# Kernel tuning notes

Measured on AMD Instinct MI355X. Metric: run time of the kernel, lower is better.

Reference implementation:

```python
import jax, jax.numpy as jnp
import numpy as np


def setup_inputs() -> dict:
    key = jax.random.key(0)
    k = jax.random.split(key, 5)
    bs, n_heads, ch, n_obj, emb = 4, 8, 64, 8, 64
    ih = iw = 32
    T = ih * iw
    return {
        "qkv": jax.random.normal(k[0], (bs, 3 * n_heads * ch, T), dtype=jnp.float32),
        "bboxes": jax.random.uniform(k[1], (bs, n_obj, 5), dtype=jnp.float32),
        "null_prompt_emb": jax.random.normal(k[2], (bs, emb, T), dtype=jnp.float32),
        "prompt_emb": jax.random.normal(k[3], (bs, emb, T), dtype=jnp.float32),
        "W_prompt": jax.random.normal(k[4], (3 * n_heads * ch, emb), dtype=jnp.float32) * 0.02,
        "n_heads": n_heads,
        "image_h": ih,
        "image_w": iw,
    }


def _region_masks(bboxes, h, w):
    # Faithful translation of get_region: bbox unpacked as (x, y, width, height, obj_idx).
    # Returns float masks [b, n_obj, h*w].
    x, y, bw, bh = bboxes[..., 0], bboxes[..., 1], bboxes[..., 2], bboxes[..., 3]
    i0 = jnp.minimum(float(h) - 1.0, jnp.floor(y * h))
    j0 = jnp.minimum(float(w) - 1.0, jnp.floor(x * w))
    i1 = i0 + jnp.maximum(1.0, jnp.ceil(bh * h))
    j1 = j0 + jnp.maximum(1.0, jnp.ceil(bw * w))
    ii = jnp.arange(h, dtype=jnp.float32)
    jj = jnp.arange(w, dtype=jnp.float32)
    mi = (ii >= i0[..., None]) & (ii < i1[..., None])          # [b, n, h]
    mj = (jj >= j0[..., None]) & (jj < j1[..., None])          # [b, n, w]
    m = (mi[..., :, None] & mj[..., None, :]).astype(jnp.float32)  # [b, n, h, w]
    return m.reshape(m.shape[0], m.shape[1], h * w)


def reference(qkv, bboxes, null_prompt_emb, prompt_emb, W_prompt, n_heads, image_h, image_w):
    bs, width, T = qkv.shape
    ch = width // (3 * n_heads)
    scale = float(ch) ** -0.25  # 1/sqrt(sqrt(ch))

    def split3(x):
        x = x.reshape(bs * n_heads, 3 * ch, T)
        return x[:, :ch], x[:, ch:2 * ch], x[:, 2 * ch:]

    q, k, v = split3(qkv)
    # to_prompt_token is a 1x1 Conv1d (no bias) == matmul over the channel dim
    nq, nk, nv = split3(jnp.einsum('oc,bct->bot', W_prompt, null_prompt_emb))
    pq, pk, pv = split3(jnp.einsum('oc,bct->bot', W_prompt, prompt_emb))

    def attn(qh, kh, vh, col_mask=None):
        w = jnp.einsum('bct,bcs->bts', qh * scale, kh * scale)
        if col_mask is not None:
            w = jnp.where(col_mask[:, None, :] > 0.5, w, -1e9)
        w = jax.nn.softmax(w.astype(jnp.float32), axis=-1).astype(qh.dtype)
        return jnp.einsum('bts,bcs->btc', w, vh)  # [bs*heads, T, ch]

    # global (null-prompt) attention
    a_null = attn(q + nq, k + nk, v + nv)

    # per-object masked attention, blended by region masks
    masks = _region_masks(bboxes, image_h, image_w)       # [bs, n_obj, T]
    masks = jnp.repeat(masks, n_heads, axis=0)            # [(bs*heads), n_obj, T]
    qf, kf, vf = q + pq, k + pk, v + pv
    a_fg = jnp.zeros_like(a_null)
    counter = jnp.zeros((bs * n_heads, T, 1), dtype=jnp.float32)
    for o in range(masks.shape[1]):  # small fixed loop over objects
        m = masks[:, o]                                   # [bs*heads, T]
        a_fg = a_fg + m[:, :, None] * attn(qf, kf, vf, col_mask=m)
        counter = counter + m[:, :, None]
    fg = counter > 0.5
    a_final = jnp.where(fg, a_fg, a_null) / jnp.where(fg, counter, 1.0)
    return jnp.transpose(a_final, (0, 2, 1)).reshape(bs, n_heads * ch, T)
```

## Files before the change

kernel.cpp:

```cpp
#include <hip/hip_runtime.h>

#define BS 4
#define NH 8
#define TT 1024
#define WROWS 1536
#define NOBJ 8
#define NT 65536

#define QNT_OFF  0
#define KNT_OFF  2097152
#define VNCS_OFF 4194304
#define QFT_OFF  6291456
#define KFT_OFF  8388608
#define VFT_OFF  10485760

typedef __attribute__((ext_vector_type(8))) short short8;
typedef __attribute__((ext_vector_type(4))) float v4f;

__device__ __forceinline__ short f2bf(float f) {
    unsigned u = __float_as_uint(f);
    u = (u + 0x7FFF + ((u >> 16) & 1)) >> 16;
    return (short)u;
}
__device__ __forceinline__ unsigned cvtpk(float a, float b) {
    unsigned u;
    asm("v_cvt_pk_bf16_f32 %0, %1, %2" : "=v"(u) : "v"(a), "v"(b));
    return u;
}
__device__ __forceinline__ float fexp2(float x) {
    float r;
    asm("v_exp_f32 %0, %1" : "=v"(r) : "v"(x));
    return r;
}
__device__ __forceinline__ int pi64(int s) { return 4 * (s & 15) + (s >> 4); }

__device__ __forceinline__ void get_region(const float* __restrict__ bb,
                                           int& i0, int& j0, int& hh, int& ww) {
    float x = bb[0], y = bb[1], bw = bb[2], bh = bb[3];
    float i0f = fminf(31.0f, floorf(y * 32.0f));
    float j0f = fminf(31.0f, floorf(x * 32.0f));
    float i1f = i0f + fmaxf(1.0f, ceilf(bh * 32.0f));
    float j1f = j0f + fmaxf(1.0f, ceilf(bw * 32.0f));
    i0 = (int)i0f; j0 = (int)j0f;
    int i1 = min(32, (int)i1f);
    int j1 = min(32, (int)j1f);
    hh = i1 - i0; ww = j1 - j0;
}

__global__ __launch_bounds__(256)
void fuse_kernel(const float* __restrict__ qkv, const float* __restrict__ nEmb,
                 const float* __restrict__ pEmb, const float* __restrict__ W,
                 short* __restrict__ wsS) {
    __shared__ float WtT[64][68];
    __shared__ float En[64][64];
    __shared__ float Ep[64][64];
    short* sbuf = (short*)&WtT[0][0];
    int t0 = blockIdx.x * 64;
    int r0 = blockIdx.y * 64;
    int b  = blockIdx.z;
    int tid = threadIdx.x;
    int half = tid >> 4;
    int q4 = (tid & 15) * 4;
#pragma unroll
    for (int p = 0; p < 4; ++p) {
        int rr = p * 16 + half;
        float4 w4 = *(const float4*)&W[(r0 + rr) * 64 + q4];
        WtT[q4 + 0][rr] = w4.x; WtT[q4 + 1][rr] = w4.y;
        WtT[q4 + 2][rr] = w4.z; WtT[q4 + 3][rr] = w4.w;
        int e = p * 16 + half;
        *(float4*)&En[e][q4] = *(const float4*)&nEmb[(b * 64 + e) * TT + t0 + q4];
        *(float4*)&Ep[e][q4] = *(const float4*)&pEmb[(b * 64 + e) * TT + t0 + q4];
    }
    __syncthreads();
    int tr = tid >> 4, tc = tid & 15;
    float an[4][4] = {{0.f}}, ap[4][4] = {{0.f}};
#pragma unroll 8
    for (int e = 0; e < 64; ++e) {
        float4 w4 = *(const float4*)&WtT[e][tr * 4];
        float4 n4 = *(const float4*)&En[e][tc * 4];
        float4 p4 = *(const float4*)&Ep[e][tc * 4];
        float w[4]  = {w4.x, w4.y, w4.z, w4.w};
        float nn[4] = {n4.x, n4.y, n4.z, n4.w};
        float pp[4] = {p4.x, p4.y, p4.z, p4.w};
#pragma unroll
        for (int i = 0; i < 4; ++i)
#pragma unroll
            for (int j = 0; j < 4; ++j) {
                an[i][j] += w[i] * nn[j];
                ap[i][j] += w[i] * pp[j];
            }
    }
    int sec = (r0 % 192) / 64;
    int h = r0 / 192, bh = b * 8 + h;
    float sc = (sec == 0) ? 0.18033688f : 1.0f;
#pragma unroll
    for (int i = 0; i < 4; ++i) {
        int r = r0 + tr * 4 + i;
        float4 x4 = *(const float4*)&qkv[(b * WROWS + r) * TT + t0 + tc * 4];
        an[i][0] = (an[i][0] + x4.x) * sc; an[i][1] = (an[i][1] + x4.y) * sc;
        an[i][2] = (an[i][2] + x4.z) * sc; an[i][3] = (an[i][3] + x4.w) * sc;
        ap[i][0] = (ap[i][0] + x4.x) * sc; ap[i][1] = (ap[i][1] + x4.y) * sc;
        ap[i][2] = (ap[i][2] + x4.z) * sc; ap[i][3] = (ap[i][3] + x4.w) * sc;
    }
    if (sec == 2) {
        short* Vn = wsS + VNCS_OFF + bh * NT;
        __syncthreads();
#pragma unroll
        for (int i = 0; i < 4; ++i)
#pragma unroll
            for (int j = 0; j < 4; ++j) {
                int p = tc * 4 + j;
                sbuf[(tr * 4 + i) * 72 + pi64(p)] = f2bf(an[i][j]);
            }
        __syncthreads();
#pragma unroll
        for (int rep = 0; rep < 2; ++rep) {
            int idx = rep * 256 + tid; int cl = idx >> 3, c8 = idx & 7;
            *(short8*)&Vn[cl * TT + t0 + c8 * 8] = *(const short8*)&sbuf[cl * 72 + c8 * 8];
        }
        short* dst = wsS + VFT_OFF + bh * NT + t0 * 64;
        __syncthreads();
#pragma unroll
        for (int j = 0; j < 4; ++j) {
            uint2 u; u.x = cvtpk(ap[0][j], ap[1][j]); u.y = cvtpk(ap[2][j], ap[3][j]);
            *(uint2*)&sbuf[(tc * 4 + j) * 72 + tr * 4] = u;
        }
        __syncthreads();
#pragma unroll
        for (int rep = 0; rep < 2; ++rep) {
            int idx = rep * 256 + tid; int tl = idx >> 3, c8 = idx & 7;
            *(short8*)&dst[tl * 64 + c8 * 8] = *(const short8*)&sbuf[tl * 72 + c8 * 8];
        }
    } else {
        short* dn = wsS + (sec == 0 ? QNT_OFF : KNT_OFF) + bh * NT + t0 * 64;
        short* df = wsS + (sec == 0 ? QFT_OFF : KFT_OFF) + bh * NT + t0 * 64;
        __syncthreads();
#pragma unroll
        for (int j = 0; j < 4; ++j) {
            uint2 u; u.x = cvtpk(an[0][j], an[1][j]); u.y = cvtpk(an[2][j], an[3][j]);
            *(uint2*)&sbuf[(tc * 4 + j) * 72 + tr * 4] = u;
        }
        __syncthreads();
#pragma unroll
        for (int rep = 0; rep < 2; ++rep) {
            int idx = rep * 256 + tid; int tl = idx >> 3, c8 = idx & 7;
            *(short8*)&dn[tl * 64 + c8 * 8] = *(const short8*)&sbuf[tl * 72 + c8 * 8];
        }
        __syncthreads();
#pragma unroll
        for (int j = 0; j < 4; ++j) {
            uint2 u; u.x = cvtpk(ap[0][j], ap[1][j]); u.y = cvtpk(ap[2][j], ap[3][j]);
            *(uint2*)&sbuf[(tc * 4 + j) * 72 + tr * 4] = u;
        }
        __syncthreads();
#pragma unroll
        for (int rep = 0; rep < 2; ++rep) {
            int idx = rep * 256 + tid; int tl = idx >> 3, c8 = idx & 7;
            *(short8*)&df[tl * 64 + c8 * 8] = *(const short8*)&sbuf[tl * 72 + c8 * 8];
        }
    }
}

__global__ __launch_bounds__(256)
void attn_fused(const short* __restrict__ wsS, const float* __restrict__ bboxes,
                float* __restrict__ out) {
    __shared__ __align__(16) short lds[13824];
    __shared__ unsigned short tmap[1024];
    short* Qs = lds;
    short* Ks = lds + 4608;
    short* Vs = lds + 9216;
    int rt = blockIdx.x, bh = blockIdx.y;
    int b = bh >> 3, h = bh & 7;
    int t0 = rt * 64;
    int tid = threadIdx.x;
    int w = tid >> 6, lane = tid & 63, ln = lane & 15, qd = lane >> 4;
    const short* QnT = wsS + QNT_OFF + bh * NT;
    const short* KnT = wsS + KNT_OFF + bh * NT;
    const short* Vn  = wsS + VNCS_OFF + bh * NT;
    const short* QfT = wsS + QFT_OFF + bh * NT;
    const short* KfT = wsS + KFT_OFF + bh * NT;
    const short* VfT = wsS + VFT_OFF + bh * NT;
    int sidx = tid, scell = sidx >> 3, sc8 = sidx & 7;
    int sidx2 = 256 + tid, scell2 = sidx2 >> 3, sc82 = sidx2 & 7;

    *(short8*)&Qs[scell * 72 + sc8 * 8]  = *(const short8*)&QnT[(t0 + scell) * 64 + sc8 * 8];
    *(short8*)&Qs[scell2 * 72 + sc82 * 8] = *(const short8*)&QnT[(t0 + scell2) * 64 + sc82 * 8];
    __syncthreads();
    short8 aq0 = *(const short8*)&Qs[(16 * w + ln) * 72 + qd * 8];
    short8 aq1 = *(const short8*)&Qs[(16 * w + ln) * 72 + 32 + qd * 8];
    v4f O[4]; float l[4];
#pragma unroll
    for (int r = 0; r < 4; ++r) l[r] = 0.f;
#pragma unroll
    for (int cc = 0; cc < 4; ++cc) O[cc] = (v4f){0.f, 0.f, 0.f, 0.f};
    short8 kreg[2], vreg[2];
    kreg[0] = *(const short8*)&KnT[scell * 64 + sc8 * 8];
    kreg[1] = *(const short8*)&KnT[scell2 * 64 + sc82 * 8];
    vreg[0] = *(const short8*)&Vn[scell * TT + sc8 * 8];
    vreg[1] = *(const short8*)&Vn[scell2 * TT + sc82 * 8];
    for (int ct = 0; ct < 16; ++ct) {
        __syncthreads();
        *(short8*)&Ks[scell * 72 + sc8 * 8]  = kreg[0];
        *(short8*)&Ks[scell2 * 72 + sc82 * 8] = kreg[1];
        *(short8*)&Vs[scell * 72 + sc8 * 8]  = vreg[0];
        *(short8*)&Vs[scell2 * 72 + sc82 * 8] = vreg[1];
        __syncthreads();
        if (ct < 15) {
            int s0 = (ct + 1) * 64;
            kreg[0] = *(const short8*)&KnT[(s0 + scell) * 64 + sc8 * 8];
            kreg[1] = *(const short8*)&KnT[(s0 + scell2) * 64 + sc82 * 8];
            vreg[0] = *(const short8*)&Vn[scell * TT + s0 + sc8 * 8];
            vreg[1] = *(const short8*)&Vn[scell2 * TT + s0 + sc82 * 8];
        }
        v4f S[4];
#pragma unroll
        for (int nn = 0; nn < 4; ++nn) {
            short8 b0 = *(const short8*)&Ks[(nn * 16 + ln) * 72 + qd * 8];
            short8 b1 = *(const short8*)&Ks[(nn * 16 + ln) * 72 + 32 + qd * 8];
            v4f z = (v4f){0.f, 0.f, 0.f, 0.f};
            z = __builtin_amdgcn_mfma_f32_16x16x32_bf16(aq0, b0, z, 0, 0, 0);
            z = __builtin_amdgcn_mfma_f32_16x16x32_bf16(aq1, b1, z, 0, 0, 0);
            S[nn] = z;
        }
#pragma unroll
        for (int r = 0; r < 4; ++r) {
            float e0 = fexp2(S[0][r]);
            float e1 = fexp2(S[1][r]);
            float e2 = fexp2(S[2][r]);
            float e3 = fexp2(S[3][r]);
            l[r] += (e0 + e1) + (e2 + e3);
            uint2 u; u.x = cvtpk(e0, e1); u.y = cvtpk(e2, e3);
            *(uint2*)&Qs[(w * 16 + 4 * qd + r) * 72 + 4 * ln] = u;
        }
        short8 ap0 = *(const short8*)&Qs[(w * 16 + ln) * 72 + qd * 8];
        short8 ap1 = *(const short8*)&Qs[(w * 16 + ln) * 72 + 32 + qd * 8];
#pragma unroll
        for (int cc = 0; cc < 4; ++cc) {
            short8 bv0 = *(const short8*)&Vs[(cc * 16 + ln) * 72 + qd * 8];
            short8 bv1 = *(const short8*)&Vs[(cc * 16 + ln) * 72 + 32 + qd * 8];
            O[cc] = __builtin_amdgcn_mfma_f32_16x16x32_bf16(ap0, bv0, O[cc], 0, 0, 0);
            O[cc] = __builtin_amdgcn_mfma_f32_16x16x32_bf16(ap1, bv1, O[cc], 0, 0, 0);
        }
    }
    v4f Onull[4];
#pragma unroll
    for (int r = 0; r < 4; ++r) {
        float rs = l[r];
        rs += __shfl_xor(rs, 1, 64);
        rs += __shfl_xor(rs, 2, 64);
        rs += __shfl_xor(rs, 4, 64);
        rs += __shfl_xor(rs, 8, 64);
        float inv = 1.0f / rs;
#pragma unroll
        for (int cc = 0; cc < 4; ++cc) Onull[cc][r] = O[cc][r] * inv;
    }

    __syncthreads();
    *(short8*)&Qs[scell * 72 + sc8 * 8]  = *(const short8*)&QfT[(t0 + scell) * 64 + sc8 * 8];
    *(short8*)&Qs[scell2 * 72 + sc82 * 8] = *(const short8*)&QfT[(t0 + scell2) * 64 + sc82 * 8];
    __syncthreads();
    aq0 = *(const short8*)&Qs[(16 * w + ln) * 72 + qd * 8];
    aq1 = *(const short8*)&Qs[(16 * w + ln) * 72 + 32 + qd * 8];
    v4f Oacc[4]; float cnt[4];
#pragma unroll
    for (int r = 0; r < 4; ++r) cnt[r] = 0.f;
#pragma unroll
    for (int cc = 0; cc < 4; ++cc) Oacc[cc] = (v4f){0.f, 0.f, 0.f, 0.f};

    for (int o = 0; o < NOBJ; ++o) {
        int i0, j0, hh, ww;
        get_region(&bboxes[(b * NOBJ + o) * 5], i0, j0, hh, ww);
        int i1 = i0 + hh;
        if (i0 > 2 * rt + 1 || i1 <= 2 * rt) continue;
        int R = hh * ww;
        for (int idx = tid; idx < R; idx += 256) {
            int ri = idx / ww; int rj = idx - ri * ww;
            tmap[idx] = (unsigned short)((i0 + ri) * 32 + j0 + rj);
        }
        __syncthreads();
#pragma unroll
        for (int r = 0; r < 4; ++r) l[r] = 0.f;
#pragma unroll
        for (int cc = 0; cc < 4; ++cc) O[cc] = (v4f){0.f, 0.f, 0.f, 0.f};
        int nct = (R + 63) >> 6;
        {
            int tA = tmap[min(scell, R - 1)];
            int tB = tmap[min(scell2, R - 1)];
            kreg[0] = *(const short8*)&KfT[tA * 64 + sc8 * 8];
            kreg[1] = *(const short8*)&KfT[tB * 64 + sc82 * 8];
            vreg[0] = *(const short8*)&VfT[tA * 64 + sc8 * 8];
            vreg[1] = *(const short8*)&VfT[tB * 64 + sc82 * 8];
        }
        int pA = pi64(scell), pB = pi64(scell2);
        for (int ct = 0; ct < nct; ++ct) {
            int sb = ct * 64;
            __syncthreads();
            *(short8*)&Ks[scell * 72 + sc8 * 8]  = kreg[0];
            *(short8*)&Ks[scell2 * 72 + sc82 * 8] = kreg[1];
#pragma unroll
            for (int jj = 0; jj < 8; ++jj) {
                int j = (jj + sc8) & 7;
                Vs[(sc8 * 8 + j) * 72 + pA] = vreg[0][j];
            }
#pragma unroll
            for (int jj = 0; jj < 8; ++jj) {
                int j = (jj + sc82) & 7;
                Vs[(sc82 * 8 + j) * 72 + pB] = vreg[1][j];
            }
            __syncthreads();
            if (ct + 1 < nct) {
                int s0 = sb + 64;
                int tA = tmap[min(s0 + scell, R - 1)];
                int tB = tmap[min(s0 + scell2, R - 1)];
                kreg[0] = *(const short8*)&KfT[tA * 64 + sc8 * 8];
                kreg[1] = *(const short8*)&KfT[tB * 64 + sc82 * 8];
                vreg[0] = *(const short8*)&VfT[tA * 64 + sc8 * 8];
                vreg[1] = *(const short8*)&VfT[tB * 64 + sc82 * 8];
            }
            v4f S[4];
#pragma unroll
            for (int nn = 0; nn < 4; ++nn) {
                short8 b0 = *(const short8*)&Ks[(nn * 16 + ln) * 72 + qd * 8];
                short8 b1 = *(const short8*)&Ks[(nn * 16 + ln) * 72 + 32 + qd * 8];
                v4f z = (v4f){0.f, 0.f, 0.f, 0.f};
                z = __builtin_amdgcn_mfma_f32_16x16x32_bf16(aq0, b0, z, 0, 0, 0);
                z = __builtin_amdgcn_mfma_f32_16x16x32_bf16(aq1, b1, z, 0, 0, 0);
                S[nn] = z;
            }
            float v0 = (sb +  0 + ln) < R ? 1.f : 0.f;
            float v1 = (sb + 16 + ln) < R ? 1.f : 0.f;
            float v2 = (sb + 32 + ln) < R ? 1.f : 0.f;
            float v3 = (sb + 48 + ln) < R ? 1.f : 0.f;
#pragma unroll
            for (int r = 0; r < 4; ++r) {
                float e0 = fexp2(S[0][r]) * v0;
                float e1 = fexp2(S[1][r]) * v1;
                float e2 = fexp2(S[2][r]) * v2;
                float e3 = fexp2(S[3][r]) * v3;
                l[r] += (e0 + e1) + (e2 + e3);
                uint2 u; u.x = cvtpk(e0, e1); u.y = cvtpk(e2, e3);
                *(uint2*)&Qs[(w * 16 + 4 * qd + r) * 72 + 4 * ln] = u;
            }
            short8 ap0 = *(const short8*)&Qs[(w * 16 + ln) * 72 + qd * 8];
            short8 ap1 = *(const short8*)&Qs[(w * 16 + ln) * 72 + 32 + qd * 8];
#pragma unroll
            for (int cc = 0; cc < 4; ++cc) {
                short8 bv0 = *(const short8*)&Vs[(cc * 16 + ln) * 72 + qd * 8];
                short8 bv1 = *(const short8*)&Vs[(cc * 16 + ln) * 72 + 32 + qd * 8];
                O[cc] = __builtin_amdgcn_mfma_f32_16x16x32_bf16(ap0, bv0, O[cc], 0, 0, 0);
                O[cc] = __builtin_amdgcn_mfma_f32_16x16x32_bf16(ap1, bv1, O[cc], 0, 0, 0);
            }
        }
#pragma unroll
        for (int r = 0; r < 4; ++r) {
            float rs = l[r];
            rs += __shfl_xor(rs, 1, 64);
            rs += __shfl_xor(rs, 2, 64);
            rs += __shfl_xor(rs, 4, 64);
            rs += __shfl_xor(rs, 8, 64);
            float inv = 1.0f / rs;
            int t = t0 + 16 * w + 4 * qd + r;
            int ti = t >> 5, tj = t & 31;
            bool in = (ti >= i0) && (ti < i1) && (tj >= j0) && (tj < j0 + ww);
            if (in) {
                cnt[r] += 1.f;
#pragma unroll
                for (int cc = 0; cc < 4; ++cc) Oacc[cc][r] += O[cc][r] * inv;
            }
        }
    }

    __syncthreads();
    float* Ot = (float*)lds;
#pragma unroll
    for (int r = 0; r < 4; ++r) {
        int tl = 16 * w + 4 * qd + r;
        float icnt = cnt[r] > 0.f ? 1.0f / cnt[r] : 0.f;
#pragma unroll
        for (int cc = 0; cc < 4; ++cc) {
            float val = cnt[r] > 0.f ? Oacc[cc][r] * icnt : Onull[cc][r];
            Ot[(cc * 16 + ln) * 68 + tl] = val;
        }
    }
    __syncthreads();
    int obase = (b * 512 + h * 64) * TT + t0;
#pragma unroll
    for (int rep = 0; rep < 4; ++rep) {
        int idx = rep * 256 + tid; int c = idx >> 4, t4 = (idx & 15) * 4;
        *(float4*)&out[obase + c * TT + t4] = *(float4*)&Ot[c * 68 + t4];
    }
}

extern "C" void kernel_launch(void* const* d_in, const int* in_sizes, int n_in,
                              void* d_out, int out_size, void* d_ws, size_t ws_size,
                              hipStream_t stream) {
    const float* qkv    = (const float*)d_in[0];
    const float* bboxes = (const float*)d_in[1];
    const float* nEmb   = (const float*)d_in[2];
    const float* pEmb   = (const float*)d_in[3];
    const float* W      = (const float*)d_in[4];
    short* wsS = (short*)d_ws;
    float* out = (float*)d_out;

    fuse_kernel<<<dim3(16, 24, 4), 256, 0, stream>>>(qkv, nEmb, pEmb, W, wsS);
    attn_fused<<<dim3(16, 32), 256, 0, stream>>>(wsS, bboxes, out);
}
```

Before: 154.4 us.

## Shrink attention tiles to one image row and load K/V fragments directly from global

Each attention block now covers 32 query tokens (one image row) with 128 threads instead of 64 tokens with 256, so the grid holds twice as many blocks. The null-prompt pass reads Q, K and V MFMA fragments straight from global memory instead of staging them in LDS, which removes the per-tile barriers. The masked object pass gathers K directly through the token map and double-buffers only the transposed V tile in LDS. The region test becomes a column-only check, since a block's tokens all lie in one row. The cost is more redundant global and L2 traffic, because each wave re-reads K and V without sharing them through LDS.

```diff
diff --git a/kernel.cpp b/kernel.cpp
--- a/kernel.cpp
+++ b/kernel.cpp
@@ -161,62 +161,45 @@
     }
 }
 
-__global__ __launch_bounds__(256)
+__global__ __launch_bounds__(128)
 void attn_fused(const short* __restrict__ wsS, const float* __restrict__ bboxes,
                 float* __restrict__ out) {
-    __shared__ __align__(16) short lds[13824];
+    __shared__ __align__(16) short lds[11520];
     __shared__ unsigned short tmap[1024];
-    short* Qs = lds;
-    short* Ks = lds + 4608;
-    short* Vs = lds + 9216;
-    int rt = blockIdx.x, bh = blockIdx.y;
+    short* Ps = lds;
+    short* Vb = lds + 2304;
+    float* Ot = (float*)(lds + 2304);
+
+    int bh = blockIdx.x, rt = blockIdx.y;
     int b = bh >> 3, h = bh & 7;
-    int t0 = rt * 64;
+    int t0 = rt * 32;
     int tid = threadIdx.x;
-    int w = tid >> 6, lane = tid & 63, ln = lane & 15, qd = lane >> 4;
+    int w = tid >> 6;
+    int lane = tid & 63, ln = lane & 15, qd = lane >> 4;
+    int rB = tid >> 3, c8 = tid & 7;
+
     const short* QnT = wsS + QNT_OFF + bh * NT;
     const short* KnT = wsS + KNT_OFF + bh * NT;
     const short* Vn  = wsS + VNCS_OFF + bh * NT;
     const short* QfT = wsS + QFT_OFF + bh * NT;
     const short* KfT = wsS + KFT_OFF + bh * NT;
     const short* VfT = wsS + VFT_OFF + bh * NT;
-    int sidx = tid, scell = sidx >> 3, sc8 = sidx & 7;
-    int sidx2 = 256 + tid, scell2 = sidx2 >> 3, sc82 = sidx2 & 7;
-
-    *(short8*)&Qs[scell * 72 + sc8 * 8]  = *(const short8*)&QnT[(t0 + scell) * 64 + sc8 * 8];
-    *(short8*)&Qs[scell2 * 72 + sc82 * 8] = *(const short8*)&QnT[(t0 + scell2) * 64 + sc82 * 8];
-    __syncthreads();
-    short8 aq0 = *(const short8*)&Qs[(16 * w + ln) * 72 + qd * 8];
-    short8 aq1 = *(const short8*)&Qs[(16 * w + ln) * 72 + 32 + qd * 8];
+
+    short8 aq0 = *(const short8*)&QnT[(t0 + 16 * w + ln) * 64 + qd * 8];
+    short8 aq1 = *(const short8*)&QnT[(t0 + 16 * w + ln) * 64 + 32 + qd * 8];
     v4f O[4]; float l[4];
 #pragma unroll
     for (int r = 0; r < 4; ++r) l[r] = 0.f;
 #pragma unroll
     for (int cc = 0; cc < 4; ++cc) O[cc] = (v4f){0.f, 0.f, 0.f, 0.f};
-    short8 kreg[2], vreg[2];
-    kreg[0] = *(const short8*)&KnT[scell * 64 + sc8 * 8];
-    kreg[1] = *(const short8*)&KnT[scell2 * 64 + sc82 * 8];
-    vreg[0] = *(const short8*)&Vn[scell * TT + sc8 * 8];
-    vreg[1] = *(const short8*)&Vn[scell2 * TT + sc82 * 8];
     for (int ct = 0; ct < 16; ++ct) {
-        __syncthreads();
-        *(short8*)&Ks[scell * 72 + sc8 * 8]  = kreg[0];
-        *(short8*)&Ks[scell2 * 72 + sc82 * 8] = kreg[1];
-        *(short8*)&Vs[scell * 72 + sc8 * 8]  = vreg[0];
-        *(short8*)&Vs[scell2 * 72 + sc82 * 8] = vreg[1];
-        __syncthreads();
-        if (ct < 15) {
-            int s0 = (ct + 1) * 64;
-            kreg[0] = *(const short8*)&KnT[(s0 + scell) * 64 + sc8 * 8];
-            kreg[1] = *(const short8*)&KnT[(s0 + scell2) * 64 + sc82 * 8];
-            vreg[0] = *(const short8*)&Vn[scell * TT + s0 + sc8 * 8];
-            vreg[1] = *(const short8*)&Vn[scell2 * TT + s0 + sc82 * 8];
-        }
+        int s0 = ct * 64;
         v4f S[4];
 #pragma unroll
         for (int nn = 0; nn < 4; ++nn) {
-            short8 b0 = *(const short8*)&Ks[(nn * 16 + ln) * 72 + qd * 8];
-            short8 b1 = *(const short8*)&Ks[(nn * 16 + ln) * 72 + 32 + qd * 8];
+            const short* kp = &KnT[(s0 + nn * 16 + ln) * 64 + qd * 8];
+            short8 b0 = *(const short8*)kp;
+            short8 b1 = *(const short8*)(kp + 32);
             v4f z = (v4f){0.f, 0.f, 0.f, 0.f};
             z = __builtin_amdgcn_mfma_f32_16x16x32_bf16(aq0, b0, z, 0, 0, 0);
             z = __builtin_amdgcn_mfma_f32_16x16x32_bf16(aq1, b1, z, 0, 0, 0);
@@ -230,14 +213,15 @@
             float e3 = fexp2(S[3][r]);
             l[r] += (e0 + e1) + (e2 + e3);
             uint2 u; u.x = cvtpk(e0, e1); u.y = cvtpk(e2, e3);
-            *(uint2*)&Qs[(w * 16 + 4 * qd + r) * 72 + 4 * ln] = u;
-        }
-        short8 ap0 = *(const short8*)&Qs[(w * 16 + ln) * 72 + qd * 8];
-        short8 ap1 = *(const short8*)&Qs[(w * 16 + ln) * 72 + 32 + qd * 8];
+            *(uint2*)&Ps[(w * 16 + 4 * qd + r) * 72 + 4 * ln] = u;
+        }
+        short8 ap0 = *(const short8*)&Ps[(w * 16 + ln) * 72 + qd * 8];
+        short8 ap1 = *(const short8*)&Ps[(w * 16 + ln) * 72 + 32 + qd * 8];
 #pragma unroll
         for (int cc = 0; cc < 4; ++cc) {
-            short8 bv0 = *(const short8*)&Vs[(cc * 16 + ln) * 72 + qd * 8];
-            short8 bv1 = *(const short8*)&Vs[(cc * 16 + ln) * 72 + 32 + qd * 8];
+            const short* vp = &Vn[(cc * 16 + ln) * TT + s0 + qd * 8];
+            short8 bv0 = *(const short8*)vp;
+            short8 bv1 = *(const short8*)(vp + 32);
             O[cc] = __builtin_amdgcn_mfma_f32_16x16x32_bf16(ap0, bv0, O[cc], 0, 0, 0);
             O[cc] = __builtin_amdgcn_mfma_f32_16x16x32_bf16(ap1, bv1, O[cc], 0, 0, 0);
         }
@@ -255,12 +239,8 @@
         for (int cc = 0; cc < 4; ++cc) Onull[cc][r] = O[cc][r] * inv;
     }
 
-    __syncthreads();
-    *(short8*)&Qs[scell * 72 + sc8 * 8]  = *(const short8*)&QfT[(t0 + scell) * 64 + sc8 * 8];
-    *(short8*)&Qs[scell2 * 72 + sc82 * 8] = *(const short8*)&QfT[(t0 + scell2) * 64 + sc82 * 8];
-    __syncthreads();
-    aq0 = *(const short8*)&Qs[(16 * w + ln) * 72 + qd * 8];
-    aq1 = *(const short8*)&Qs[(16 * w + ln) * 72 + 32 + qd * 8];
+    aq0 = *(const short8*)&QfT[(t0 + 16 * w + ln) * 64 + qd * 8];
+    aq1 = *(const short8*)&QfT[(t0 + 16 * w + ln) * 64 + 32 + qd * 8];
     v4f Oacc[4]; float cnt[4];
 #pragma unroll
     for (int r = 0; r < 4; ++r) cnt[r] = 0.f;
@@ -271,9 +251,9 @@
         int i0, j0, hh, ww;
         get_region(&bboxes[(b * NOBJ + o) * 5], i0, j0, hh, ww);
         int i1 = i0 + hh;
-        if (i0 > 2 * rt + 1 || i1 <= 2 * rt) continue;
+        if (i0 > rt || i1 <= rt) continue;
         int R = hh * ww;
-        for (int idx = tid; idx < R; idx += 256) {
+        for (int idx = tid; idx < R; idx += 128) {
             int ri = idx / ww; int rj = idx - ri * ww;
             tmap[idx] = (unsigned short)((i0 + ri) * 32 + j0 + rj);
         }
@@ -283,45 +263,53 @@
 #pragma unroll
         for (int cc = 0; cc < 4; ++cc) O[cc] = (v4f){0.f, 0.f, 0.f, 0.f};
         int nct = (R + 63) >> 6;
-        {
-            int tA = tmap[min(scell, R - 1)];
-            int tB = tmap[min(scell2, R - 1)];
-            kreg[0] = *(const short8*)&KfT[tA * 64 + sc8 * 8];
-            kreg[1] = *(const short8*)&KfT[tB * 64 + sc82 * 8];
-            vreg[0] = *(const short8*)&VfT[tA * 64 + sc8 * 8];
-            vreg[1] = *(const short8*)&VfT[tB * 64 + sc82 * 8];
-        }
-        int pA = pi64(scell), pB = pi64(scell2);
-        for (int ct = 0; ct < nct; ++ct) {
-            int sb = ct * 64;
-            __syncthreads();
-            *(short8*)&Ks[scell * 72 + sc8 * 8]  = kreg[0];
-            *(short8*)&Ks[scell2 * 72 + sc82 * 8] = kreg[1];
+        short8 vreg[4];
+#pragma unroll
+        for (int k = 0; k < 4; ++k)
+            vreg[k] = *(const short8*)&VfT[(int)tmap[min(rB + 16 * k, R - 1)] * 64 + c8 * 8];
+#pragma unroll
+        for (int k = 0; k < 4; ++k) {
+            int pK = 4 * rB + k;
 #pragma unroll
             for (int jj = 0; jj < 8; ++jj) {
-                int j = (jj + sc8) & 7;
-                Vs[(sc8 * 8 + j) * 72 + pA] = vreg[0][j];
-            }
-#pragma unroll
-            for (int jj = 0; jj < 8; ++jj) {
-                int j = (jj + sc82) & 7;
-                Vs[(sc82 * 8 + j) * 72 + pB] = vreg[1][j];
-            }
-            __syncthreads();
-            if (ct + 1 < nct) {
-                int s0 = sb + 64;
-                int tA = tmap[min(s0 + scell, R - 1)];
-                int tB = tmap[min(s0 + scell2, R - 1)];
-                kreg[0] = *(const short8*)&KfT[tA * 64 + sc8 * 8];
-                kreg[1] = *(const short8*)&KfT[tB * 64 + sc82 * 8];
-                vreg[0] = *(const short8*)&VfT[tA * 64 + sc8 * 8];
-                vreg[1] = *(const short8*)&VfT[tB * 64 + sc82 * 8];
+                int j = (jj + c8) & 7;
+                Vb[(c8 * 8 + j) * 72 + pK] = vreg[k][j];
+            }
+        }
+        if (nct > 1) {
+#pragma unroll
+            for (int k = 0; k < 4; ++k)
+                vreg[k] = *(const short8*)&VfT[(int)tmap[min(64 + rB + 16 * k, R - 1)] * 64 + c8 * 8];
+        }
+        __syncthreads();
+        for (int p = 0; p < nct; ++p) {
+            int sb = p * 64;
+            const short* curV = Vb + (p & 1) * 4608;
+            if (p + 1 < nct) {
+                short* nxtV = Vb + ((p + 1) & 1) * 4608;
+#pragma unroll
+                for (int k = 0; k < 4; ++k) {
+                    int pK = 4 * rB + k;
+#pragma unroll
+                    for (int jj = 0; jj < 8; ++jj) {
+                        int j = (jj + c8) & 7;
+                        nxtV[(c8 * 8 + j) * 72 + pK] = vreg[k][j];
+                    }
+                }
+            }
+            if (p + 2 < nct) {
+                int s0 = sb + 128;
+#pragma unroll
+                for (int k = 0; k < 4; ++k)
+                    vreg[k] = *(const short8*)&VfT[(int)tmap[min(s0 + rB + 16 * k, R - 1)] * 64 + c8 * 8];
             }
             v4f S[4];
 #pragma unroll
             for (int nn = 0; nn < 4; ++nn) {
-                short8 b0 = *(const short8*)&Ks[(nn * 16 + ln) * 72 + qd * 8];
-                short8 b1 = *(const short8*)&Ks[(nn * 16 + ln) * 72 + 32 + qd * 8];
+                int tg = tmap[min(sb + nn * 16 + ln, R - 1)];
+                const short* kp = &KfT[tg * 64 + qd * 8];
+                short8 b0 = *(const short8*)kp;
+                short8 b1 = *(const short8*)(kp + 32);
                 v4f z = (v4f){0.f, 0.f, 0.f, 0.f};
                 z = __builtin_amdgcn_mfma_f32_16x16x32_bf16(aq0, b0, z, 0, 0, 0);
                 z = __builtin_amdgcn_mfma_f32_16x16x32_bf16(aq1, b1, z, 0, 0, 0);
@@ -339,17 +327,18 @@
                 float e3 = fexp2(S[3][r]) * v3;
                 l[r] += (e0 + e1) + (e2 + e3);
                 uint2 u; u.x = cvtpk(e0, e1); u.y = cvtpk(e2, e3);
-                *(uint2*)&Qs[(w * 16 + 4 * qd + r) * 72 + 4 * ln] = u;
-            }
-            short8 ap0 = *(const short8*)&Qs[(w * 16 + ln) * 72 + qd * 8];
-            short8 ap1 = *(const short8*)&Qs[(w * 16 + ln) * 72 + 32 + qd * 8];
+                *(uint2*)&Ps[(w * 16 + 4 * qd + r) * 72 + 4 * ln] = u;
+            }
+            short8 ap0 = *(const short8*)&Ps[(w * 16 + ln) * 72 + qd * 8];
+            short8 ap1 = *(const short8*)&Ps[(w * 16 + ln) * 72 + 32 + qd * 8];
 #pragma unroll
             for (int cc = 0; cc < 4; ++cc) {
-                short8 bv0 = *(const short8*)&Vs[(cc * 16 + ln) * 72 + qd * 8];
-                short8 bv1 = *(const short8*)&Vs[(cc * 16 + ln) * 72 + 32 + qd * 8];
+                short8 bv0 = *(const short8*)&curV[(cc * 16 + ln) * 72 + qd * 8];
+                short8 bv1 = *(const short8*)&curV[(cc * 16 + ln) * 72 + 32 + qd * 8];
                 O[cc] = __builtin_amdgcn_mfma_f32_16x16x32_bf16(ap0, bv0, O[cc], 0, 0, 0);
                 O[cc] = __builtin_amdgcn_mfma_f32_16x16x32_bf16(ap1, bv1, O[cc], 0, 0, 0);
             }
+            __syncthreads();
         }
 #pragma unroll
         for (int r = 0; r < 4; ++r) {
@@ -359,9 +348,8 @@
             rs += __shfl_xor(rs, 4, 64);
             rs += __shfl_xor(rs, 8, 64);
             float inv = 1.0f / rs;
-            int t = t0 + 16 * w + 4 * qd + r;
-            int ti = t >> 5, tj = t & 31;
-            bool in = (ti >= i0) && (ti < i1) && (tj >= j0) && (tj < j0 + ww);
+            int tj = (16 * w + 4 * qd + r) & 31;
+            bool in = (tj >= j0) && (tj < j0 + ww);
             if (in) {
                 cnt[r] += 1.f;
 #pragma unroll
@@ -371,7 +359,6 @@
     }
 
     __syncthreads();
-    float* Ot = (float*)lds;
 #pragma unroll
     for (int r = 0; r < 4; ++r) {
         int tl = 16 * w + 4 * qd + r;
@@ -379,15 +366,15 @@
 #pragma unroll
         for (int cc = 0; cc < 4; ++cc) {
             float val = cnt[r] > 0.f ? Oacc[cc][r] * icnt : Onull[cc][r];
-            Ot[(cc * 16 + ln) * 68 + tl] = val;
+            Ot[(cc * 16 + ln) * 36 + tl] = val;
         }
     }
     __syncthreads();
     int obase = (b * 512 + h * 64) * TT + t0;
 #pragma unroll
     for (int rep = 0; rep < 4; ++rep) {
-        int idx = rep * 256 + tid; int c = idx >> 4, t4 = (idx & 15) * 4;
-        *(float4*)&out[obase + c * TT + t4] = *(float4*)&Ot[c * 68 + t4];
+        int idx = rep * 128 + tid; int c = idx >> 3, t4 = (idx & 7) * 4;
+        *(float4*)&out[obase + c * TT + t4] = *(float4*)&Ot[c * 36 + t4];
     }
 }
 
@@ -403,5 +390,5 @@
     float* out = (float*)d_out;
 
     fuse_kernel<<<dim3(16, 24, 4), 256, 0, stream>>>(qkv, nEmb, pEmb, W, wsS);
-    attn_fused<<<dim3(16, 32), 256, 0, stream>>>(wsS, bboxes, out);
-}
+    attn_fused<<<dim3(32, 32), 128, 0, stream>>>(wsS, bboxes, out);
+}
```

Measured after the change: 213.8 us. +38.5%, slower.
